# Kernel optimization log

Measured on AMD Instinct MI355X. Metric: run time of the kernel, lower is better.

## Reference

```python
import jax, jax.numpy as jnp
import numpy as np

SMOOTH = 1e-05
N_SCALES = 3
# 3x3 cross-shaped boundary kernel, OIHW layout [1,1,3,3]
_KERNEL = jnp.array([[0., 1., 0.], [1., 1., 1.], [0., 1., 0.]], jnp.float32).reshape(1, 1, 3, 3)


def _nearest_ds(t, h, w):
    """torch F.interpolate mode='nearest': src_idx = floor(dst_idx * in/out)."""
    H, W = t.shape[-2], t.shape[-1]
    ih = (jnp.arange(h) * H) // h
    iw = (jnp.arange(w) * W) // w
    return t[..., ih[:, None], iw[None, :]]


def _boundary_dou(probs, tgt, valid):
    # probs, tgt: [B,N,h,w] float32; valid: [B,N] float32 in {0,1}
    B, N, h, w = probs.shape
    Y = jax.lax.conv_general_dilated(
        tgt.reshape(B * N, 1, h, w), _KERNEL,
        window_strides=(1, 1), padding=[(1, 1), (1, 1)],
        dimension_numbers=('NCHW', 'OIHW', 'NCHW')).reshape(B, N, h, w)
    Y = Y * tgt
    Y = jnp.where(Y == 5.0, 0.0, Y)  # interior pixels zeroed, boundary kept
    C = jnp.sum(Y != 0, axis=(-2, -1)).astype(jnp.float32)   # [B,N] boundary count
    S = jnp.sum(tgt != 0, axis=(-2, -1)).astype(jnp.float32)  # [B,N] fg count
    alpha = 2.0 * (1.0 - (C + SMOOTH) / (S + SMOOTH)) - 1.0
    alpha = jnp.minimum(alpha, 0.8)
    inter = jnp.sum(probs * tgt, axis=(-2, -1))
    y_sum = jnp.sum(tgt * tgt, axis=(-2, -1))
    z_sum = jnp.sum(probs * probs, axis=(-2, -1))
    dou = (z_sum + y_sum - 2.0 * inter + SMOOTH) / (z_sum + y_sum - (1.0 + alpha) * inter + SMOOTH)
    per = jnp.where(S > 0, dou, probs.mean(axis=(-2, -1)))  # empty-target fallback
    cnt = valid.sum()
    return jnp.where(cnt > 0, (per * valid).sum() / cnt, 0.0)


def reference(logits0, logits1, logits2, targets, valid_mask):
    outs = [logits0, logits1, logits2]
    ws = np.array([1.0 / 2.0 ** i for i in range(N_SCALES)])
    ws = ws / ws.sum()  # nnU-Net deep supervision weights
    tgt_full = targets.astype(jnp.float32)
    valid = (valid_mask >= 0.5).astype(jnp.float32)
    loss = jnp.float32(0.0)
    for w_i, out in zip(ws, outs):
        h, w = out.shape[-2], out.shape[-1]
        tgt = _nearest_ds(tgt_full, h, w)
        probs = jax.nn.sigmoid(out.astype(jnp.float32))
        loss = loss + jnp.float32(w_i) * _boundary_dou(probs, tgt, valid)
    return loss


def setup_inputs() -> dict:
    key = jax.random.key(0)
    k0, k1, k2, kt = jax.random.split(key, 4)
    B, N = 8, 4
    return {
        'logits0': jax.random.normal(k0, (B, N, 512, 512), jnp.float32),
        'logits1': jax.random.normal(k1, (B, N, 256, 256), jnp.float32),
        'logits2': jax.random.normal(k2, (B, N, 128, 128), jnp.float32),
        'targets': jax.random.randint(kt, (B, N, 512, 512), 0, 2, jnp.int32),
        'valid_mask': jnp.ones((B, N), jnp.float32),
    }
```

## Files before the change

### kernel.cpp

```cpp
#include <hip/hip_runtime.h>

#define SMOOTH 1e-5f


__device__ __forceinline__ float wave_reduce(float v) {
#pragma unroll
    for (int off = 32; off; off >>= 1) v += __shfl_down(v, off, 64);
    return v;
}

__device__ __forceinline__ float sigmoidf(float x) {
    return 1.f / (1.f + __expf(-x));
}

__global__ __launch_bounds__(256) void bdou_fused(
    const float* __restrict__ l0, const float* __restrict__ l1,
    const float* __restrict__ l2, const int* __restrict__ tgt,
    float* __restrict__ ws)
{
    __shared__ unsigned Tw[72 * 20];
    __shared__ float red[4][15];

    const int blk  = blockIdx.x;
    const int img  = (blk & 7) + 8 * (blk >> 9);
    const int tile = (blk >> 3) & 63;
    const int ty0  = (tile >> 3) * 64;
    const int tx0  = (tile & 7) * 64;
    const int tid  = threadIdx.x;

    const int* __restrict__ timg = tgt + (size_t)img * (512 * 512);

    for (int j = tid; j < 1296; j += 256) {
        int r = j / 18, c = j - r * 18;
        int gy = ty0 - 4 + r;
        int gx = tx0 - 4 + c * 4;
        unsigned w = 0;
        if ((unsigned)gy < 512u && (unsigned)gx < 512u) {
            int4 v = *reinterpret_cast<const int4*>(timg + (size_t)gy * 512 + gx);
            w = (v.x != 0 ? 1u : 0) | (v.y != 0 ? 1u << 8 : 0) |
                (v.z != 0 ? 1u << 16 : 0) | (v.w != 0 ? 1u << 24 : 0);
        }
        Tw[r * 20 + c] = w;
    }
    __syncthreads();

    int   cC0 = 0, cS0 = 0, cC1 = 0, cS1 = 0, cC2 = 0, cS2 = 0;
    float aI0 = 0.f, aZ0 = 0.f, aP0 = 0.f;
    float aI1 = 0.f, aZ1 = 0.f, aP1 = 0.f;
    float aI2 = 0.f, aZ2 = 0.f, aP2 = 0.f;

    {
        const float* __restrict__ l0img = l0 + (size_t)img * (512 * 512);
#pragma unroll
        for (int it = 0; it < 4; ++it) {
            int p  = tid * 4 + it * 1024;
            int ly = p >> 6, lx = p & 63;
            float4 lg = *reinterpret_cast<const float4*>(
                l0img + (size_t)(ty0 + ly) * 512 + tx0 + lx);
            int wb = lx >> 2;
            unsigned cw = Tw[(ly + 4) * 20 + wb + 1];
            unsigned lw = Tw[(ly + 4) * 20 + wb];
            unsigned rw = Tw[(ly + 4) * 20 + wb + 2];
            unsigned uw = Tw[(ly + 3) * 20 + wb + 1];
            unsigned dw = Tw[(ly + 5) * 20 + wb + 1];
            float pr[4] = {sigmoidf(lg.x), sigmoidf(lg.y), sigmoidf(lg.z), sigmoidf(lg.w)};
#pragma unroll
            for (int j = 0; j < 4; ++j) {
                unsigned t = (cw >> (8 * j)) & 1u;
                unsigned u = (uw >> (8 * j)) & 1u;
                unsigned d = (dw >> (8 * j)) & 1u;
                unsigned lf = (j == 0) ? (lw >> 24) & 1u : (cw >> (8 * (j - 1))) & 1u;
                unsigned rt = (j == 3) ? rw & 1u : (cw >> (8 * (j + 1))) & 1u;
                cS0 += (int)t;
                cC0 += (int)(t & ~(u & d & lf & rt));
                aI0 += pr[j] * (float)t;
                aZ0 += pr[j] * pr[j];
                aP0 += pr[j];
            }
        }
    }

    {
        int dY = tid >> 3, dXb = (tid & 7) * 4;
        int fy = dY * 2, fx = (tid & 7) * 8;
        float4 lg = *reinterpret_cast<const float4*>(
            l1 + (size_t)img * 65536 + (size_t)(ty0 / 2 + dY) * 256 + tx0 / 2 + dXb);
        int rb = (fy + 4) * 20 + (fx >> 2);
        unsigned cwv[4] = {Tw[rb], Tw[rb + 1], Tw[rb + 2], Tw[rb + 3]};
        unsigned uwv[2] = {Tw[rb - 40 + 1], Tw[rb - 40 + 2]};
        unsigned dwv[2] = {Tw[rb + 40 + 1], Tw[rb + 40 + 2]};
        float pr[4] = {sigmoidf(lg.x), sigmoidf(lg.y), sigmoidf(lg.z), sigmoidf(lg.w)};
#pragma unroll
        for (int j = 0; j < 4; ++j) {
            unsigned t  = (cwv[(2 + j) >> 1] >> (16 * ((2 + j) & 1))) & 1u;
            unsigned lf = (cwv[(1 + j) >> 1] >> (16 * ((1 + j) & 1))) & 1u;
            unsigned rt = (cwv[(3 + j) >> 1] >> (16 * ((3 + j) & 1))) & 1u;
            unsigned u  = (uwv[((2 + j) >> 1) - 1] >> (16 * ((2 + j) & 1))) & 1u;
            unsigned d  = (dwv[((2 + j) >> 1) - 1] >> (16 * ((2 + j) & 1))) & 1u;
            cS1 += (int)t;
            cC1 += (int)(t & ~(u & d & lf & rt));
            aI1 += pr[j] * (float)t;
            aZ1 += pr[j] * pr[j];
            aP1 += pr[j];
        }
    }

    {
        int dY = tid >> 4, dX = tid & 15;
        int fy = dY * 4, fx = dX * 4;
        const unsigned char* Tb = (const unsigned char*)Tw;
        int rc = (fy + 4) * 80 + fx + 4;
        unsigned t  = Tb[rc];
        unsigned u  = Tb[rc - 4 * 80];
        unsigned d  = Tb[rc + 4 * 80];
        unsigned lf = Tb[rc - 4];
        unsigned rt = Tb[rc + 4];
        float lg = l2[(size_t)img * 16384 + (size_t)(ty0 / 4 + dY) * 128 + tx0 / 4 + dX];
        float pr = sigmoidf(lg);
        cS2 += (int)t;
        cC2 += (int)(t & ~(u & d & lf & rt));
        aI2 += pr * (float)t;
        aZ2 += pr * pr;
        aP2 += pr;
    }

    float vals[15] = {(float)cC0, (float)cS0, aI0, aZ0, aP0,
                      (float)cC1, (float)cS1, aI1, aZ1, aP1,
                      (float)cC2, (float)cS2, aI2, aZ2, aP2};
#pragma unroll
    for (int k = 0; k < 15; ++k) vals[k] = wave_reduce(vals[k]);
    int wave = tid >> 6, lane = tid & 63;
    if (lane == 0) {
#pragma unroll
        for (int k = 0; k < 15; ++k) red[wave][k] = vals[k];
    }
    __syncthreads();
    if (tid < 15) {
        float s = red[0][tid] + red[1][tid] + red[2][tid] + red[3][tid];
        int sc = tid / 5, k = tid - sc * 5;
        atomicAdd(&ws[(sc * 32 + img) * 5 + k], s);
    }
}

__global__ void bdou_final(const float* __restrict__ ws,
                           const float* __restrict__ valid_mask,
                           float* __restrict__ out)
{
    int tid = threadIdx.x;
    float contrib = 0.f, cpart = 0.f;
    if (tid < 96) {
        int s = tid >> 5, i = tid & 31;
        const float* w = ws + tid * 5;
        float C = w[0], S = w[1], I = w[2], Z = w[3], P = w[4];
        float valid = (valid_mask[i] >= 0.5f) ? 1.f : 0.f;
        float alpha = fminf(2.f * (1.f - (C + SMOOTH) / (S + SMOOTH)) - 1.f, 0.8f);
        float dou = (Z + S - 2.f * I + SMOOTH) /
                    (Z + S - (1.f + alpha) * I + SMOOTH);
        const float wts[3]  = {4.f / 7.f, 2.f / 7.f, 1.f / 7.f};
        const float pixc[3] = {262144.f, 65536.f, 16384.f};
        float per = (S > 0.f) ? dou : (P / pixc[s]);
        contrib = wts[s] * per * valid;
        if (tid < 32) cpart = valid;
    }
    contrib = wave_reduce(contrib);
    cpart   = wave_reduce(cpart);
    __shared__ float sm[2][2];
    int wv = tid >> 6, ln = tid & 63;
    if (ln == 0) { sm[wv][0] = contrib; sm[wv][1] = cpart; }
    __syncthreads();
    if (tid == 0) {
        float tot = sm[0][0] + sm[1][0];
        float cnt = sm[0][1] + sm[1][1];
        out[0] = (cnt > 0.f) ? tot / cnt : 0.f;
    }
}

extern "C" void kernel_launch(void* const* d_in, const int* in_sizes, int n_in,
                              void* d_out, int out_size, void* d_ws, size_t ws_size,
                              hipStream_t stream) {
    const float* l0 = (const float*)d_in[0];
    const float* l1 = (const float*)d_in[1];
    const float* l2 = (const float*)d_in[2];
    const int*   tg = (const int*)d_in[3];
    const float* vm = (const float*)d_in[4];
    float* ws = (float*)d_ws;

    hipMemsetAsync(ws, 0, 3 * 32 * 5 * sizeof(float), stream);
    bdou_fused<<<2048, 256, 0, stream>>>(l0, l1, l2, tg, ws);
    bdou_final<<<1, 128, 0, stream>>>(ws, vm, (float*)d_out);
}
```

Baseline: 117.5 us.

## Replace LDS tile stencil with row-strip wave-per-row bitmask stencil using shuffles

```diff
diff --git a/kernel.cpp b/kernel.cpp
--- a/kernel.cpp
+++ b/kernel.cpp
@@ -1,6 +1,9 @@
 #include <hip/hip_runtime.h>
 
 #define SMOOTH 1e-5f
+
+typedef float floatx4 __attribute__((ext_vector_type(4)));
+typedef float floatx2 __attribute__((ext_vector_type(2)));
 
 
 __device__ __forceinline__ float wave_reduce(float v) {
@@ -13,126 +16,149 @@
     return 1.f / (1.f + __expf(-x));
 }
 
-__global__ __launch_bounds__(256) void bdou_fused(
+__device__ __forceinline__ unsigned pack8(int4 a, int4 b) {
+    return (unsigned)(a.x != 0)        | ((unsigned)(a.y != 0) << 1) |
+           ((unsigned)(a.z != 0) << 2) | ((unsigned)(a.w != 0) << 3) |
+           ((unsigned)(b.x != 0) << 4) | ((unsigned)(b.y != 0) << 5) |
+           ((unsigned)(b.z != 0) << 6) | ((unsigned)(b.w != 0) << 7);
+}
+__device__ __forceinline__ unsigned even4(unsigned b) {
+    return (b & 1u) | ((b >> 1) & 2u) | ((b >> 2) & 4u) | ((b >> 3) & 8u);
+}
+__device__ __forceinline__ unsigned ext2(unsigned b) {
+    return (b & 1u) | ((b >> 3) & 2u);
+}
+
+template<int W>
+__device__ __forceinline__ int stencil_cnt(unsigned u, unsigned c, unsigned d, int lane)
+{
+    unsigned pv = __shfl_up(c, 1);
+    unsigned nx = __shfl_down(c, 1);
+    if (lane == 0)  pv = 0;
+    if (lane == 63) nx = 0;
+    const unsigned M = (1u << W) - 1u;
+    unsigned lv = ((c << 1) | ((pv >> (W - 1)) & 1u)) & M;
+    unsigned rv = ((c >> 1) | ((nx & 1u) << (W - 1))) & M;
+    return __popc(c & ~(u & d & lv & rv));
+}
+
+__device__ __forceinline__ void acc_row8(floatx4 a, floatx4 b, unsigned bits,
+                                         float& I, float& Z, float& P) {
+    float pr[8] = {sigmoidf(a.x), sigmoidf(a.y), sigmoidf(a.z), sigmoidf(a.w),
+                   sigmoidf(b.x), sigmoidf(b.y), sigmoidf(b.z), sigmoidf(b.w)};
+#pragma unroll
+    for (int j = 0; j < 8; ++j) {
+        I += ((bits >> j) & 1u) ? pr[j] : 0.f;
+        Z += pr[j] * pr[j];
+        P += pr[j];
+    }
+}
+__device__ __forceinline__ void acc_row4(floatx4 a, unsigned bits,
+                                         float& I, float& Z, float& P) {
+    float pr[4] = {sigmoidf(a.x), sigmoidf(a.y), sigmoidf(a.z), sigmoidf(a.w)};
+#pragma unroll
+    for (int j = 0; j < 4; ++j) {
+        I += ((bits >> j) & 1u) ? pr[j] : 0.f;
+        Z += pr[j] * pr[j];
+        P += pr[j];
+    }
+}
+__device__ __forceinline__ void acc_row2(floatx2 a, unsigned bits,
+                                         float& I, float& Z, float& P) {
+    float pr[2] = {sigmoidf(a.x), sigmoidf(a.y)};
+#pragma unroll
+    for (int j = 0; j < 2; ++j) {
+        I += ((bits >> j) & 1u) ? pr[j] : 0.f;
+        Z += pr[j] * pr[j];
+        P += pr[j];
+    }
+}
+
+__global__ __launch_bounds__(256) void bdou_unified(
     const float* __restrict__ l0, const float* __restrict__ l1,
     const float* __restrict__ l2, const int* __restrict__ tgt,
     float* __restrict__ ws)
 {
-    __shared__ unsigned Tw[72 * 20];
-    __shared__ float red[4][15];
-
     const int blk  = blockIdx.x;
-    const int img  = (blk & 7) + 8 * (blk >> 9);
-    const int tile = (blk >> 3) & 63;
-    const int ty0  = (tile >> 3) * 64;
-    const int tx0  = (tile & 7) * 64;
     const int tid  = threadIdx.x;
-
-    const int* __restrict__ timg = tgt + (size_t)img * (512 * 512);
-
-    for (int j = tid; j < 1296; j += 256) {
-        int r = j / 18, c = j - r * 18;
-        int gy = ty0 - 4 + r;
-        int gx = tx0 - 4 + c * 4;
-        unsigned w = 0;
-        if ((unsigned)gy < 512u && (unsigned)gx < 512u) {
-            int4 v = *reinterpret_cast<const int4*>(timg + (size_t)gy * 512 + gx);
-            w = (v.x != 0 ? 1u : 0) | (v.y != 0 ? 1u << 8 : 0) |
-                (v.z != 0 ? 1u << 16 : 0) | (v.w != 0 ? 1u << 24 : 0);
-        }
-        Tw[r * 20 + c] = w;
-    }
-    __syncthreads();
-
-    int   cC0 = 0, cS0 = 0, cC1 = 0, cS1 = 0, cC2 = 0, cS2 = 0;
+    const int w    = tid >> 6, lane = tid & 63;
+    const int img  = blk >> 5;
+    const int y0   = (blk & 31) * 16 + w * 4;
+
+    const int*   T  = tgt + (size_t)img * 262144 + lane * 8;
+    const float* L0 = l0  + (size_t)img * 262144 + lane * 8;
+    const float* L1 = l1  + (size_t)img * 65536  + lane * 4;
+    const float* L2 = l2  + (size_t)img * 16384  + lane * 2;
+
+    const int ym4 = (y0 >= 4) ? y0 - 4 : 0;
+    const int ym2 = (y0 >= 2) ? y0 - 2 : 0;
+    const int ym1 = (y0 >= 1) ? y0 - 1 : 0;
+    const int yp4 = (y0 + 4 <= 511) ? y0 + 4 : 511;
+    const unsigned mu = (y0 > 0)   ? 0xFFu : 0u;
+    const unsigned md = (y0 < 508) ? 0xFFu : 0u;
+
+    int4 tA0 = *(const int4*)(T + (size_t)ym4 * 512), tA1 = *(const int4*)(T + (size_t)ym4 * 512 + 4);
+    int4 tB0 = *(const int4*)(T + (size_t)ym2 * 512), tB1 = *(const int4*)(T + (size_t)ym2 * 512 + 4);
+    int4 tC0 = *(const int4*)(T + (size_t)ym1 * 512), tC1 = *(const int4*)(T + (size_t)ym1 * 512 + 4);
+    int4 t00 = *(const int4*)(T + (size_t)(y0    ) * 512), t01 = *(const int4*)(T + (size_t)(y0    ) * 512 + 4);
+    int4 t10 = *(const int4*)(T + (size_t)(y0 + 1) * 512), t11 = *(const int4*)(T + (size_t)(y0 + 1) * 512 + 4);
+    int4 t20 = *(const int4*)(T + (size_t)(y0 + 2) * 512), t21 = *(const int4*)(T + (size_t)(y0 + 2) * 512 + 4);
+    int4 t30 = *(const int4*)(T + (size_t)(y0 + 3) * 512), t31 = *(const int4*)(T + (size_t)(y0 + 3) * 512 + 4);
+    int4 tD0 = *(const int4*)(T + (size_t)yp4 * 512), tD1 = *(const int4*)(T + (size_t)yp4 * 512 + 4);
+    floatx4 g00 = *(const floatx4*)(L0 + (size_t)(y0    ) * 512), g01 = *(const floatx4*)(L0 + (size_t)(y0    ) * 512 + 4);
+    floatx4 g10 = *(const floatx4*)(L0 + (size_t)(y0 + 1) * 512), g11 = *(const floatx4*)(L0 + (size_t)(y0 + 1) * 512 + 4);
+    floatx4 g20 = *(const floatx4*)(L0 + (size_t)(y0 + 2) * 512), g21 = *(const floatx4*)(L0 + (size_t)(y0 + 2) * 512 + 4);
+    floatx4 g30 = *(const floatx4*)(L0 + (size_t)(y0 + 3) * 512), g31 = *(const floatx4*)(L0 + (size_t)(y0 + 3) * 512 + 4);
+    floatx4 h0  = *(const floatx4*)(L1 + (size_t)(y0 / 2    ) * 256);
+    floatx4 h1  = *(const floatx4*)(L1 + (size_t)(y0 / 2 + 1) * 256);
+    floatx2 q0  = *(const floatx2*)(L2 + (size_t)(y0 / 4) * 128);
+
+    unsigned bm4 = pack8(tA0, tA1) & mu;
+    unsigned bm2 = pack8(tB0, tB1) & mu;
+    unsigned bm1 = pack8(tC0, tC1) & mu;
+    unsigned b0  = pack8(t00, t01);
+    unsigned b1  = pack8(t10, t11);
+    unsigned b2  = pack8(t20, t21);
+    unsigned b3  = pack8(t30, t31);
+    unsigned bp4 = pack8(tD0, tD1) & md;
+
+    int cC0, cS0, cC1, cS1, cC2, cS2;
     float aI0 = 0.f, aZ0 = 0.f, aP0 = 0.f;
     float aI1 = 0.f, aZ1 = 0.f, aP1 = 0.f;
     float aI2 = 0.f, aZ2 = 0.f, aP2 = 0.f;
 
+    cS0 = __popc(b0) + __popc(b1) + __popc(b2) + __popc(b3);
+    cC0 = stencil_cnt<8>(bm1, b0, b1, lane) + stencil_cnt<8>(b0, b1, b2, lane) +
+          stencil_cnt<8>(b1, b2, b3, lane) + stencil_cnt<8>(b2, b3, bp4, lane);
+    acc_row8(g00, g01, b0, aI0, aZ0, aP0);
+    acc_row8(g10, g11, b1, aI0, aZ0, aP0);
+    acc_row8(g20, g21, b2, aI0, aZ0, aP0);
+    acc_row8(g30, g31, b3, aI0, aZ0, aP0);
+
     {
-        const float* __restrict__ l0img = l0 + (size_t)img * (512 * 512);
-#pragma unroll
-        for (int it = 0; it < 4; ++it) {
-            int p  = tid * 4 + it * 1024;
-            int ly = p >> 6, lx = p & 63;
-            float4 lg = *reinterpret_cast<const float4*>(
-                l0img + (size_t)(ty0 + ly) * 512 + tx0 + lx);
-            int wb = lx >> 2;
-            unsigned cw = Tw[(ly + 4) * 20 + wb + 1];
-            unsigned lw = Tw[(ly + 4) * 20 + wb];
-            unsigned rw = Tw[(ly + 4) * 20 + wb + 2];
-            unsigned uw = Tw[(ly + 3) * 20 + wb + 1];
-            unsigned dw = Tw[(ly + 5) * 20 + wb + 1];
-            float pr[4] = {sigmoidf(lg.x), sigmoidf(lg.y), sigmoidf(lg.z), sigmoidf(lg.w)};
-#pragma unroll
-            for (int j = 0; j < 4; ++j) {
-                unsigned t = (cw >> (8 * j)) & 1u;
-                unsigned u = (uw >> (8 * j)) & 1u;
-                unsigned d = (dw >> (8 * j)) & 1u;
-                unsigned lf = (j == 0) ? (lw >> 24) & 1u : (cw >> (8 * (j - 1))) & 1u;
-                unsigned rt = (j == 3) ? rw & 1u : (cw >> (8 * (j + 1))) & 1u;
-                cS0 += (int)t;
-                cC0 += (int)(t & ~(u & d & lf & rt));
-                aI0 += pr[j] * (float)t;
-                aZ0 += pr[j] * pr[j];
-                aP0 += pr[j];
-            }
-        }
+        unsigned cu = even4(bm2), c0 = even4(b0), c1 = even4(b2), cd = even4(bp4);
+        cS1 = __popc(c0) + __popc(c1);
+        cC1 = stencil_cnt<4>(cu, c0, c1, lane) + stencil_cnt<4>(c0, c1, cd, lane);
+        acc_row4(h0, c0, aI1, aZ1, aP1);
+        acc_row4(h1, c1, aI1, aZ1, aP1);
     }
 
     {
-        int dY = tid >> 3, dXb = (tid & 7) * 4;
-        int fy = dY * 2, fx = (tid & 7) * 8;
-        float4 lg = *reinterpret_cast<const float4*>(
-            l1 + (size_t)img * 65536 + (size_t)(ty0 / 2 + dY) * 256 + tx0 / 2 + dXb);
-        int rb = (fy + 4) * 20 + (fx >> 2);
-        unsigned cwv[4] = {Tw[rb], Tw[rb + 1], Tw[rb + 2], Tw[rb + 3]};
-        unsigned uwv[2] = {Tw[rb - 40 + 1], Tw[rb - 40 + 2]};
-        unsigned dwv[2] = {Tw[rb + 40 + 1], Tw[rb + 40 + 2]};
-        float pr[4] = {sigmoidf(lg.x), sigmoidf(lg.y), sigmoidf(lg.z), sigmoidf(lg.w)};
-#pragma unroll
-        for (int j = 0; j < 4; ++j) {
-            unsigned t  = (cwv[(2 + j) >> 1] >> (16 * ((2 + j) & 1))) & 1u;
-            unsigned lf = (cwv[(1 + j) >> 1] >> (16 * ((1 + j) & 1))) & 1u;
-            unsigned rt = (cwv[(3 + j) >> 1] >> (16 * ((3 + j) & 1))) & 1u;
-            unsigned u  = (uwv[((2 + j) >> 1) - 1] >> (16 * ((2 + j) & 1))) & 1u;
-            unsigned d  = (dwv[((2 + j) >> 1) - 1] >> (16 * ((2 + j) & 1))) & 1u;
-            cS1 += (int)t;
-            cC1 += (int)(t & ~(u & d & lf & rt));
-            aI1 += pr[j] * (float)t;
-            aZ1 += pr[j] * pr[j];
-            aP1 += pr[j];
-        }
-    }
-
-    {
-        int dY = tid >> 4, dX = tid & 15;
-        int fy = dY * 4, fx = dX * 4;
-        const unsigned char* Tb = (const unsigned char*)Tw;
-        int rc = (fy + 4) * 80 + fx + 4;
-        unsigned t  = Tb[rc];
-        unsigned u  = Tb[rc - 4 * 80];
-        unsigned d  = Tb[rc + 4 * 80];
-        unsigned lf = Tb[rc - 4];
-        unsigned rt = Tb[rc + 4];
-        float lg = l2[(size_t)img * 16384 + (size_t)(ty0 / 4 + dY) * 128 + tx0 / 4 + dX];
-        float pr = sigmoidf(lg);
-        cS2 += (int)t;
-        cC2 += (int)(t & ~(u & d & lf & rt));
-        aI2 += pr * (float)t;
-        aZ2 += pr * pr;
-        aP2 += pr;
+        unsigned zu = ext2(bm4), z = ext2(b0), zd = ext2(bp4);
+        cS2 = __popc(z);
+        cC2 = stencil_cnt<2>(zu, z, zd, lane);
+        acc_row2(q0, z, aI2, aZ2, aP2);
     }
 
     float vals[15] = {(float)cC0, (float)cS0, aI0, aZ0, aP0,
                       (float)cC1, (float)cS1, aI1, aZ1, aP1,
                       (float)cC2, (float)cS2, aI2, aZ2, aP2};
+    __shared__ float red[4][15];
 #pragma unroll
     for (int k = 0; k < 15; ++k) vals[k] = wave_reduce(vals[k]);
-    int wave = tid >> 6, lane = tid & 63;
     if (lane == 0) {
 #pragma unroll
-        for (int k = 0; k < 15; ++k) red[wave][k] = vals[k];
+        for (int k = 0; k < 15; ++k) red[w][k] = vals[k];
     }
     __syncthreads();
     if (tid < 15) {
@@ -185,7 +211,7 @@
     const float* vm = (const float*)d_in[4];
     float* ws = (float*)d_ws;
 
-    hipMemsetAsync(ws, 0, 3 * 32 * 5 * sizeof(float), stream);
-    bdou_fused<<<2048, 256, 0, stream>>>(l0, l1, l2, tg, ws);
+    (void)hipMemsetAsync(ws, 0, 3 * 32 * 5 * sizeof(float), stream);
+    bdou_unified<<<1024, 256, 0, stream>>>(l0, l1, l2, tg, ws);
     bdou_final<<<1, 128, 0, stream>>>(ws, vm, (float*)d_out);
 }
```

New measurement: 111.7 us. -4.9%, faster.
